# Optimization experiments

Measured on AMD Instinct MI355X. Metric: run time of the kernel, lower is better.

Reference implementation:

```python
import jax, jax.numpy as jnp
import numpy as np

N = 65536
WAVE_SPEED = 1.0


def _mlp(pt, Ws, bs):
    # pt: [4] -> scalar. 6 tanh hidden layers of width 128, linear head.
    h = pt
    for W, b in zip(Ws[:-1], bs[:-1]):
        h = jnp.tanh(W @ h + b)
    return (Ws[-1] @ h + bs[-1])[0]


def setup_inputs() -> dict:
    key = jax.random.key(0)
    ks = jax.random.split(key, 32)
    d = {}
    for i, name in enumerate(["t", "x", "y", "z"]):
        d[name] = jax.random.normal(ks[i], (N,), dtype=jnp.float32)
    sizes = [(128, 4)] + [(128, 128)] * 5 + [(1, 128)]
    for i, (fan_out, fan_in) in enumerate(sizes):
        # Glorot-like scale for tanh MLP
        scale = np.float32(1.0 / np.sqrt(fan_in))
        d[f"W{i}"] = jax.random.normal(ks[4 + i], (fan_out, fan_in), dtype=jnp.float32) * scale
        d[f"b{i}"] = jnp.zeros((fan_out,), dtype=jnp.float32)
    return d


def reference(t, x, y, z, W0, b0, W1, b1, W2, b2, W3, b3, W4, b4, W5, b5, W6, b6):
    Ws = [W0, W1, W2, W3, W4, W5, W6]
    bs = [b0, b1, b2, b3, b4, b5, b6]

    def u(pt):
        return _mlp(pt, Ws, bs)

    def residual_point(pt):
        # Full 4x4 Hessian via forward-over-reverse; we need only the diagonal.
        H = jax.hessian(u)(pt)  # [4, 4]
        u_tt = H[0, 0]
        laplacian = H[1, 1] + H[2, 2] + H[3, 3]
        return u_tt - (WAVE_SPEED ** 2) * laplacian

    pts = jnp.stack([t, x, y, z], axis=-1)  # [N, 4]
    return jax.vmap(residual_point)(pts)  # [N]
```

## Files before the change

kernel.cpp:

```cpp
#include <hip/hip_runtime.h>
#include <hip/hip_fp16.h>
#include <math.h>


typedef _Float16 f16x8 __attribute__((ext_vector_type(8)));
typedef _Float16 f16x4 __attribute__((ext_vector_type(4)));
typedef _Float16 f16x2 __attribute__((ext_vector_type(2)));
typedef float    f32x4 __attribute__((ext_vector_type(4)));

constexpr int TPB  = 256;
constexpr int P    = 16;
constexpr int H    = 128;
constexpr int NV   = 6;
constexpr int XFRAG_HALVES = NV * 4 * 64 * 8;
constexpr int WFRAG_HALVES = 5 * 8 * 4 * 64 * 8;
constexpr size_t WS_NEEDED = 2 * WFRAG_HALVES * sizeof(_Float16);

__device__ __forceinline__ float fast_tanh(float v) {
    float e = __expf(-2.0f * fabsf(v));
    float r = __builtin_amdgcn_rcpf(1.0f + e);
    return copysignf((1.0f - e) * r, v);
}

__device__ __forceinline__ f16x2 pkrtz(float a, float b) {
    return __builtin_bit_cast(f16x2, __builtin_amdgcn_cvt_pkrtz(a, b));
}

__global__ __launch_bounds__(256) void presplit_w(
    const float* __restrict__ W1, const float* __restrict__ W2,
    const float* __restrict__ W3, const float* __restrict__ W4,
    const float* __restrict__ W5, _Float16* __restrict__ whi,
    _Float16* __restrict__ wlo)
{
    const int gid = blockIdx.x * 256 + threadIdx.x;
    const float* Ws[5] = { W1, W2, W3, W4, W5 };
    const int lane = gid & 63;
    const int rest = gid >> 6;
    const int ks   = rest & 3;
    const int mt   = (rest >> 2) & 7;
    const int l    = rest >> 5;
    const int n    = mt * 16 + (lane & 15);
    const int k0   = ks * 32 + (lane >> 4) * 8;
    const float4 u0 = *(const float4*)&Ws[l][n * H + k0];
    const float4 u1 = *(const float4*)&Ws[l][n * H + k0 + 4];
    const float vv[8] = { u0.x, u0.y, u0.z, u0.w, u1.x, u1.y, u1.z, u1.w };
    f16x8 h, o;
    #pragma unroll
    for (int e = 0; e < 8; ++e) {
        _Float16 hh = (_Float16)vv[e];
        h[e] = hh;
        o[e] = (_Float16)(vv[e] - (float)hh);
    }
    *(f16x8*)&whi[gid * 8] = h;
    *(f16x8*)&wlo[gid * 8] = o;
}

__global__ __launch_bounds__(TPB, 3) void pinn_mfma8(
    const float* __restrict__ t, const float* __restrict__ x,
    const float* __restrict__ y, const float* __restrict__ z,
    const float* __restrict__ W0, const float* __restrict__ b0,
    const float* __restrict__ W1, const float* __restrict__ b1,
    const float* __restrict__ W2, const float* __restrict__ b2,
    const float* __restrict__ W3, const float* __restrict__ b3,
    const float* __restrict__ W4, const float* __restrict__ b4,
    const float* __restrict__ W5, const float* __restrict__ b5,
    const float* __restrict__ W6,
    const _Float16* __restrict__ whi, const _Float16* __restrict__ wlo,
    int use_pre, float* __restrict__ out, int N)
{
    __shared__ _Float16 sXhi[XFRAG_HALVES];
    __shared__ _Float16 sXlo[XFRAG_HALVES];
    __shared__ float    sRed[4][P];

    const int tid  = threadIdx.x;
    const int lane = tid & 63;
    const int wn   = tid >> 6;
    const int l15  = lane & 15;
    const int l4   = lane >> 4;
    const int gb   = blockIdx.x * P;

    {
        const int p0 = tid >> 4;
        const int i0 = tid & 15;
        int gp = gb + p0; if (gp >= N) gp = N - 1;
        const float pt0 = t[gp], pt1 = x[gp], pt2 = y[gp], pt3 = z[gp];
        float nv[NV][8];
        #pragma unroll
        for (int j = 0; j < 8; ++j) {
            const int i = i0 * 8 + j;
            const float4 wv = *(const float4*)&W0[i * 4];
            const float zv = fmaf(wv.x, pt0, fmaf(wv.y, pt1, fmaf(wv.z, pt2, fmaf(wv.w, pt3, b0[i]))));
            const float hv = fast_tanh(zv);
            const float s  = 1.0f - hv * hv;
            const float ssq = ((wv.x * wv.x - wv.y * wv.y) - wv.z * wv.z) - wv.w * wv.w;
            nv[0][j] = hv;       nv[1][j] = s * wv.x; nv[2][j] = s * wv.y;
            nv[3][j] = s * wv.z; nv[4][j] = s * wv.w; nv[5][j] = -2.0f * hv * s * ssq;
        }
        #pragma unroll
        for (int v = 0; v < NV; ++v) {
            f16x8 hh, oo;
            #pragma unroll
            for (int j = 0; j < 8; ++j) {
                _Float16 h_ = (_Float16)nv[v][j];
                hh[j] = h_;
                oo[j] = (_Float16)(nv[v][j] - (float)h_);
            }
            const int off = ((v * 4 + (i0 >> 2)) * 64 + p0 + 16 * (i0 & 3)) * 8;
            *(f16x8*)&sXhi[off] = hh;
            *(f16x8*)&sXlo[off] = oo;
        }
    }
    __syncthreads();

    for (int l = 0; l < 5; ++l) {
        f32x4 acc[NV][2];
        #pragma unroll
        for (int v = 0; v < NV; ++v)
            #pragma unroll
            for (int nt = 0; nt < 2; ++nt) acc[v][nt] = (f32x4){0.f, 0.f, 0.f, 0.f};

        const float* __restrict__ Wc =
            (l == 0) ? W1 : (l == 1) ? W2 : (l == 2) ? W3 : (l == 3) ? W4 : W5;

        #pragma unroll
        for (int ks = 0; ks < 4; ++ks) {
            f16x8 ah[2], al[2];
            if (use_pre) {
                #pragma unroll
                for (int nt = 0; nt < 2; ++nt) {
                    const int f = ((l * 8 + (wn * 2 + nt)) * 4 + ks) * 64 + lane;
                    ah[nt] = *(const f16x8*)&whi[f * 8];
                    al[nt] = *(const f16x8*)&wlo[f * 8];
                }
            } else {
                #pragma unroll
                for (int nt = 0; nt < 2; ++nt) {
                    const int n  = (wn * 2 + nt) * 16 + l15;
                    const int k0 = ks * 32 + l4 * 8;
                    const float4 u0 = *(const float4*)&Wc[n * H + k0];
                    const float4 u1 = *(const float4*)&Wc[n * H + k0 + 4];
                    const float vv[8] = { u0.x, u0.y, u0.z, u0.w, u1.x, u1.y, u1.z, u1.w };
                    #pragma unroll
                    for (int e = 0; e < 8; ++e) {
                        _Float16 h_ = (_Float16)vv[e];
                        ah[nt][e] = h_;
                        al[nt][e] = (_Float16)(vv[e] - (float)h_);
                    }
                }
            }
            f16x8 xh[NV], xl[NV];
            #pragma unroll
            for (int v = 0; v < NV; ++v) {
                const int base = ((v * 4 + ks) * 64 + lane) * 8;
                xh[v] = *(const f16x8*)&sXhi[base];
                xl[v] = *(const f16x8*)&sXlo[base];
            }
            __builtin_amdgcn_s_setprio(1);
            #pragma unroll
            for (int v = 0; v < NV; ++v)
                #pragma unroll
                for (int nt = 0; nt < 2; ++nt)
                    acc[v][nt] = __builtin_amdgcn_mfma_f32_16x16x32_f16(ah[nt], xh[v], acc[v][nt], 0, 0, 0);
            #pragma unroll
            for (int v = 0; v < NV; ++v)
                #pragma unroll
                for (int nt = 0; nt < 2; ++nt)
                    acc[v][nt] = __builtin_amdgcn_mfma_f32_16x16x32_f16(ah[nt], xl[v], acc[v][nt], 0, 0, 0);
            #pragma unroll
            for (int v = 0; v < NV; ++v)
                #pragma unroll
                for (int nt = 0; nt < 2; ++nt)
                    acc[v][nt] = __builtin_amdgcn_mfma_f32_16x16x32_f16(al[nt], xh[v], acc[v][nt], 0, 0, 0);
            __builtin_amdgcn_s_setprio(0);
        }
        __syncthreads();

        if (l < 4) {
            const float* __restrict__ bc =
                (l == 0) ? b1 : (l == 1) ? b2 : (l == 2) ? b3 : b4;
            #pragma unroll
            for (int nt = 0; nt < 2; ++nt) {
                const int n0  = (wn * 2 + nt) * 16 + l4 * 4;
                const int ksp = n0 >> 5;
                const int l4p = (n0 & 31) >> 3;
                const int e0  = n0 & 7;
                const float4 b4v = *(const float4*)&bc[n0];
                const float bb[4] = { b4v.x, b4v.y, b4v.z, b4v.w };
                float nv[NV][4];
                #pragma unroll
                for (int r = 0; r < 4; ++r) {
                    const float zv = acc[0][nt][r] + bb[r];
                    const float hv = fast_tanh(zv);
                    const float s  = 1.0f - hv * hv;
                    const float d0 = acc[1][nt][r], d1 = acc[2][nt][r];
                    const float d2 = acc[3][nt][r], d3 = acc[4][nt][r];
                    const float ssq = ((d0 * d0 - d1 * d1) - d2 * d2) - d3 * d3;
                    const float qn  = fmaf(s, acc[5][nt][r], -2.0f * hv * s * ssq);
                    nv[0][r] = hv;     nv[1][r] = s * d0; nv[2][r] = s * d1;
                    nv[3][r] = s * d2; nv[4][r] = s * d3; nv[5][r] = qn;
                }
                #pragma unroll
                for (int v = 0; v < NV; ++v) {
                    const f16x2 h01 = pkrtz(nv[v][0], nv[v][1]);
                    const f16x2 h23 = pkrtz(nv[v][2], nv[v][3]);
                    const float o0 = nv[v][0] - (float)h01[0];
                    const float o1 = nv[v][1] - (float)h01[1];
                    const float o2 = nv[v][2] - (float)h23[0];
                    const float o3 = nv[v][3] - (float)h23[1];
                    const f16x2 o01 = pkrtz(o0, o1);
                    const f16x2 o23 = pkrtz(o2, o3);
                    const int off = ((v * 4 + ksp) * 64 + l15 + 16 * l4p) * 8 + e0;
                    *(f16x4*)&sXhi[off] = __builtin_shufflevector(h01, h23, 0, 1, 2, 3);
                    *(f16x4*)&sXlo[off] = __builtin_shufflevector(o01, o23, 0, 1, 2, 3);
                }
            }
            __syncthreads();
        } else {
            float part = 0.0f;
            #pragma unroll
            for (int nt = 0; nt < 2; ++nt) {
                const int n0 = (wn * 2 + nt) * 16 + l4 * 4;
                const float4 b4v = *(const float4*)&b5[n0];
                const float4 w6v = *(const float4*)&W6[n0];
                const float bb[4] = { b4v.x, b4v.y, b4v.z, b4v.w };
                const float ww[4] = { w6v.x, w6v.y, w6v.z, w6v.w };
                #pragma unroll
                for (int r = 0; r < 4; ++r) {
                    const float zv = acc[0][nt][r] + bb[r];
                    const float hv = fast_tanh(zv);
                    const float s  = 1.0f - hv * hv;
                    const float d0 = acc[1][nt][r], d1 = acc[2][nt][r];
                    const float d2 = acc[3][nt][r], d3 = acc[4][nt][r];
                    const float ssq = ((d0 * d0 - d1 * d1) - d2 * d2) - d3 * d3;
                    const float qf  = fmaf(s, acc[5][nt][r], -2.0f * hv * s * ssq);
                    part = fmaf(ww[r], qf, part);
                }
            }
            part += __shfl_xor(part, 16, 64);
            part += __shfl_xor(part, 32, 64);
            if (lane < 16) sRed[wn][lane] = part;
        }
    }

    __syncthreads();
    if (tid < P) {
        const float rsum = sRed[0][tid] + sRed[1][tid] + sRed[2][tid] + sRed[3][tid];
        const int o = gb + tid;
        if (o < N) out[o] = rsum;
    }
}

extern "C" void kernel_launch(void* const* d_in, const int* in_sizes, int n_in,
                              void* d_out, int out_size, void* d_ws, size_t ws_size,
                              hipStream_t stream) {
    const float* t  = (const float*)d_in[0];
    const float* x  = (const float*)d_in[1];
    const float* y  = (const float*)d_in[2];
    const float* z  = (const float*)d_in[3];
    const float* W0 = (const float*)d_in[4];
    const float* b0 = (const float*)d_in[5];
    const float* W1 = (const float*)d_in[6];
    const float* b1 = (const float*)d_in[7];
    const float* W2 = (const float*)d_in[8];
    const float* b2 = (const float*)d_in[9];
    const float* W3 = (const float*)d_in[10];
    const float* b3 = (const float*)d_in[11];
    const float* W4 = (const float*)d_in[12];
    const float* b4 = (const float*)d_in[13];
    const float* W5 = (const float*)d_in[14];
    const float* b5 = (const float*)d_in[15];
    const float* W6 = (const float*)d_in[16];

    const int N = in_sizes[0];
    float* out = (float*)d_out;

    const int use_pre = (ws_size >= WS_NEEDED) ? 1 : 0;
    _Float16* whi = (_Float16*)d_ws;
    _Float16* wlo = whi + WFRAG_HALVES;

    if (use_pre) {
        presplit_w<<<(5 * 8 * 4 * 64) / 256, 256, 0, stream>>>(W1, W2, W3, W4, W5, whi, wlo);
    }
    const int grid = (N + P - 1) / P;
    pinn_mfma8<<<grid, TPB, 0, stream>>>(
        t, x, y, z, W0, b0, W1, b1, W2, b2, W3, b3, W4, b4, W5, b5, W6,
        whi, wlo, use_pre, out, N);
}
```

Measured before the change: 177.1 us.

## Pack two points' tangent vectors per MFMA column to halve blocks' accumulators

Each block now handles 8 points instead of 16. The six per-point tangent vectors (value, four first derivatives, second-derivative term) are interleaved so that each 16-wide MFMA N-tile holds 3 tiles × 2 channels per point, with even and odd columns carrying different channels. The cross-channel terms are recombined through lane-pair shuffles. This cuts the accumulator count from 12 to 6 f32x4, which frees registers and raises occupancy, with launch bounds going from 3 to 5 blocks per SIMD. The cost is twice as many blocks, which reload the weights more often per point, plus extra shuffles and select logic in the epilogue.

```diff
diff --git a/kernel.cpp b/kernel.cpp
--- a/kernel.cpp
+++ b/kernel.cpp
@@ -9,10 +9,11 @@
 typedef float    f32x4 __attribute__((ext_vector_type(4)));
 
 constexpr int TPB  = 256;
-constexpr int P    = 16;
+constexpr int P    = 8;
 constexpr int H    = 128;
 constexpr int NV   = 6;
-constexpr int XFRAG_HALVES = NV * 4 * 64 * 8;
+constexpr int NT   = 3;
+constexpr int XFRAG_HALVES = NT * 4 * 64 * 8;
 constexpr int WFRAG_HALVES = 5 * 8 * 4 * 64 * 8;
 constexpr size_t WS_NEEDED = 2 * WFRAG_HALVES * sizeof(_Float16);
 
@@ -55,7 +56,7 @@
     *(f16x8*)&wlo[gid * 8] = o;
 }
 
-__global__ __launch_bounds__(TPB, 3) void pinn_mfma8(
+__global__ __launch_bounds__(TPB, 5) void pinn_mfma10(
     const float* __restrict__ t, const float* __restrict__ x,
     const float* __restrict__ y, const float* __restrict__ z,
     const float* __restrict__ W0, const float* __restrict__ b0,
@@ -77,17 +78,18 @@
     const int wn   = tid >> 6;
     const int l15  = lane & 15;
     const int l4   = lane >> 4;
+    const int vo   = lane & 1;
     const int gb   = blockIdx.x * P;
 
     {
-        const int p0 = tid >> 4;
-        const int i0 = tid & 15;
+        const int p0 = tid >> 5;
+        const int i0 = tid & 31;
         int gp = gb + p0; if (gp >= N) gp = N - 1;
         const float pt0 = t[gp], pt1 = x[gp], pt2 = y[gp], pt3 = z[gp];
-        float nv[NV][8];
-        #pragma unroll
-        for (int j = 0; j < 8; ++j) {
-            const int i = i0 * 8 + j;
+        float nv[NV][4];
+        #pragma unroll
+        for (int j = 0; j < 4; ++j) {
+            const int i = i0 * 4 + j;
             const float4 wv = *(const float4*)&W0[i * 4];
             const float zv = fmaf(wv.x, pt0, fmaf(wv.y, pt1, fmaf(wv.z, pt2, fmaf(wv.w, pt3, b0[i]))));
             const float hv = fast_tanh(zv);
@@ -98,26 +100,28 @@
         }
         #pragma unroll
         for (int v = 0; v < NV; ++v) {
-            f16x8 hh, oo;
-            #pragma unroll
-            for (int j = 0; j < 8; ++j) {
+            f16x4 hh, oo;
+            #pragma unroll
+            for (int j = 0; j < 4; ++j) {
                 _Float16 h_ = (_Float16)nv[v][j];
                 hh[j] = h_;
                 oo[j] = (_Float16)(nv[v][j] - (float)h_);
             }
-            const int off = ((v * 4 + (i0 >> 2)) * 64 + p0 + 16 * (i0 & 3)) * 8;
-            *(f16x8*)&sXhi[off] = hh;
-            *(f16x8*)&sXlo[off] = oo;
+            const int off = (((v >> 1) * 4 + (i0 >> 3)) * 64
+                             + 16 * ((i0 >> 1) & 3) + 2 * p0 + (v & 1)) * 8
+                            + (i0 & 1) * 4;
+            *(f16x4*)&sXhi[off] = hh;
+            *(f16x4*)&sXlo[off] = oo;
         }
     }
     __syncthreads();
 
     for (int l = 0; l < 5; ++l) {
-        f32x4 acc[NV][2];
-        #pragma unroll
-        for (int v = 0; v < NV; ++v)
-            #pragma unroll
-            for (int nt = 0; nt < 2; ++nt) acc[v][nt] = (f32x4){0.f, 0.f, 0.f, 0.f};
+        f32x4 acc[NT][2];
+        #pragma unroll
+        for (int nt = 0; nt < NT; ++nt)
+            #pragma unroll
+            for (int m = 0; m < 2; ++m) acc[nt][m] = (f32x4){0.f, 0.f, 0.f, 0.f};
 
         const float* __restrict__ Wc =
             (l == 0) ? W1 : (l == 1) ? W2 : (l == 2) ? W3 : (l == 3) ? W4 : W5;
@@ -127,15 +131,15 @@
             f16x8 ah[2], al[2];
             if (use_pre) {
                 #pragma unroll
-                for (int nt = 0; nt < 2; ++nt) {
-                    const int f = ((l * 8 + (wn * 2 + nt)) * 4 + ks) * 64 + lane;
-                    ah[nt] = *(const f16x8*)&whi[f * 8];
-                    al[nt] = *(const f16x8*)&wlo[f * 8];
+                for (int m = 0; m < 2; ++m) {
+                    const int f = ((l * 8 + (wn * 2 + m)) * 4 + ks) * 64 + lane;
+                    ah[m] = *(const f16x8*)&whi[f * 8];
+                    al[m] = *(const f16x8*)&wlo[f * 8];
                 }
             } else {
                 #pragma unroll
-                for (int nt = 0; nt < 2; ++nt) {
-                    const int n  = (wn * 2 + nt) * 16 + l15;
+                for (int m = 0; m < 2; ++m) {
+                    const int n  = (wn * 2 + m) * 16 + l15;
                     const int k0 = ks * 32 + l4 * 8;
                     const float4 u0 = *(const float4*)&Wc[n * H + k0];
                     const float4 u1 = *(const float4*)&Wc[n * H + k0 + 4];
@@ -143,34 +147,34 @@
                     #pragma unroll
                     for (int e = 0; e < 8; ++e) {
                         _Float16 h_ = (_Float16)vv[e];
-                        ah[nt][e] = h_;
-                        al[nt][e] = (_Float16)(vv[e] - (float)h_);
+                        ah[m][e] = h_;
+                        al[m][e] = (_Float16)(vv[e] - (float)h_);
                     }
                 }
             }
-            f16x8 xh[NV], xl[NV];
-            #pragma unroll
-            for (int v = 0; v < NV; ++v) {
-                const int base = ((v * 4 + ks) * 64 + lane) * 8;
-                xh[v] = *(const f16x8*)&sXhi[base];
-                xl[v] = *(const f16x8*)&sXlo[base];
+            f16x8 xh[NT], xl[NT];
+            #pragma unroll
+            for (int nt = 0; nt < NT; ++nt) {
+                const int base = ((nt * 4 + ks) * 64 + lane) * 8;
+                xh[nt] = *(const f16x8*)&sXhi[base];
+                xl[nt] = *(const f16x8*)&sXlo[base];
             }
             __builtin_amdgcn_s_setprio(1);
             #pragma unroll
-            for (int v = 0; v < NV; ++v)
-                #pragma unroll
-                for (int nt = 0; nt < 2; ++nt)
-                    acc[v][nt] = __builtin_amdgcn_mfma_f32_16x16x32_f16(ah[nt], xh[v], acc[v][nt], 0, 0, 0);
-            #pragma unroll
-            for (int v = 0; v < NV; ++v)
-                #pragma unroll
-                for (int nt = 0; nt < 2; ++nt)
-                    acc[v][nt] = __builtin_amdgcn_mfma_f32_16x16x32_f16(ah[nt], xl[v], acc[v][nt], 0, 0, 0);
-            #pragma unroll
-            for (int v = 0; v < NV; ++v)
-                #pragma unroll
-                for (int nt = 0; nt < 2; ++nt)
-                    acc[v][nt] = __builtin_amdgcn_mfma_f32_16x16x32_f16(al[nt], xh[v], acc[v][nt], 0, 0, 0);
+            for (int nt = 0; nt < NT; ++nt)
+                #pragma unroll
+                for (int m = 0; m < 2; ++m)
+                    acc[nt][m] = __builtin_amdgcn_mfma_f32_16x16x32_f16(ah[m], xh[nt], acc[nt][m], 0, 0, 0);
+            #pragma unroll
+            for (int nt = 0; nt < NT; ++nt)
+                #pragma unroll
+                for (int m = 0; m < 2; ++m)
+                    acc[nt][m] = __builtin_amdgcn_mfma_f32_16x16x32_f16(ah[m], xl[nt], acc[nt][m], 0, 0, 0);
+            #pragma unroll
+            for (int nt = 0; nt < NT; ++nt)
+                #pragma unroll
+                for (int m = 0; m < 2; ++m)
+                    acc[nt][m] = __builtin_amdgcn_mfma_f32_16x16x32_f16(al[m], xh[nt], acc[nt][m], 0, 0, 0);
             __builtin_amdgcn_s_setprio(0);
         }
         __syncthreads();
@@ -179,66 +183,73 @@
             const float* __restrict__ bc =
                 (l == 0) ? b1 : (l == 1) ? b2 : (l == 2) ? b3 : b4;
             #pragma unroll
-            for (int nt = 0; nt < 2; ++nt) {
-                const int n0  = (wn * 2 + nt) * 16 + l4 * 4;
-                const int ksp = n0 >> 5;
-                const int l4p = (n0 & 31) >> 3;
-                const int e0  = n0 & 7;
-                const float4 b4v = *(const float4*)&bc[n0];
-                const float bb[4] = { b4v.x, b4v.y, b4v.z, b4v.w };
-                float nv[NV][4];
+            for (int m = 0; m < 2; ++m) {
+                float o0[4], o1[4], o2[4];
                 #pragma unroll
                 for (int r = 0; r < 4; ++r) {
-                    const float zv = acc[0][nt][r] + bb[r];
-                    const float hv = fast_tanh(zv);
-                    const float s  = 1.0f - hv * hv;
-                    const float d0 = acc[1][nt][r], d1 = acc[2][nt][r];
-                    const float d2 = acc[3][nt][r], d3 = acc[4][nt][r];
-                    const float ssq = ((d0 * d0 - d1 * d1) - d2 * d2) - d3 * d3;
-                    const float qn  = fmaf(s, acc[5][nt][r], -2.0f * hv * s * ssq);
-                    nv[0][r] = hv;     nv[1][r] = s * d0; nv[2][r] = s * d1;
-                    nv[3][r] = s * d2; nv[4][r] = s * d3; nv[5][r] = qn;
-                }
-                #pragma unroll
-                for (int v = 0; v < NV; ++v) {
-                    const f16x2 h01 = pkrtz(nv[v][0], nv[v][1]);
-                    const f16x2 h23 = pkrtz(nv[v][2], nv[v][3]);
-                    const float o0 = nv[v][0] - (float)h01[0];
-                    const float o1 = nv[v][1] - (float)h01[1];
-                    const float o2 = nv[v][2] - (float)h23[0];
-                    const float o3 = nv[v][3] - (float)h23[1];
-                    const f16x2 o01 = pkrtz(o0, o1);
-                    const f16x2 o23 = pkrtz(o2, o3);
-                    const int off = ((v * 4 + ksp) * 64 + l15 + 16 * l4p) * 8 + e0;
+                    const int n  = (wn * 2 + m) * 16 + l4 * 4 + r;
+                    const float a0 = acc[0][m][r];
+                    const float a1 = acc[1][m][r];
+                    const float a2 = acc[2][m][r];
+                    const float hv  = fast_tanh(a0 + bc[n]);
+                    const float s   = 1.0f - hv * hv;
+                    const float ue  = a1 * a1 + a2 * a2;
+                    const float hs2 = 2.0f * hv * s;
+                    const float s_x   = __shfl_xor(s, 1, 64);
+                    const float hs2_x = __shfl_xor(hs2, 1, 64);
+                    const float ue_x  = __shfl_xor(ue, 1, 64);
+                    const float uo  = a0 * a0 - a1 * a1;
+                    const float ssq = uo - ue_x;
+                    const float qn  = fmaf(s_x, a2, -hs2_x * ssq);
+                    o0[r] = vo ? s_x * a0 : hv;
+                    o1[r] = vo ? s_x * a1 : s * a1;
+                    o2[r] = vo ? qn       : s * a2;
+                }
+                const int wbase = 16 * (2 * m + (l4 >> 1)) + l15;
+                const int e0    = (l4 & 1) * 4;
+                #pragma unroll
+                for (int nt = 0; nt < NT; ++nt) {
+                    const float* ov = (nt == 0) ? o0 : (nt == 1) ? o1 : o2;
+                    const f16x2 h01 = pkrtz(ov[0], ov[1]);
+                    const f16x2 h23 = pkrtz(ov[2], ov[3]);
+                    const float q0 = ov[0] - (float)h01[0];
+                    const float q1 = ov[1] - (float)h01[1];
+                    const float q2 = ov[2] - (float)h23[0];
+                    const float q3 = ov[3] - (float)h23[1];
+                    const f16x2 g01 = pkrtz(q0, q1);
+                    const f16x2 g23 = pkrtz(q2, q3);
+                    const int off = ((nt * 4 + wn) * 64 + wbase) * 8 + e0;
                     *(f16x4*)&sXhi[off] = __builtin_shufflevector(h01, h23, 0, 1, 2, 3);
-                    *(f16x4*)&sXlo[off] = __builtin_shufflevector(o01, o23, 0, 1, 2, 3);
+                    *(f16x4*)&sXlo[off] = __builtin_shufflevector(g01, g23, 0, 1, 2, 3);
                 }
             }
             __syncthreads();
         } else {
             float part = 0.0f;
             #pragma unroll
-            for (int nt = 0; nt < 2; ++nt) {
-                const int n0 = (wn * 2 + nt) * 16 + l4 * 4;
-                const float4 b4v = *(const float4*)&b5[n0];
-                const float4 w6v = *(const float4*)&W6[n0];
-                const float bb[4] = { b4v.x, b4v.y, b4v.z, b4v.w };
-                const float ww[4] = { w6v.x, w6v.y, w6v.z, w6v.w };
+            for (int m = 0; m < 2; ++m) {
                 #pragma unroll
                 for (int r = 0; r < 4; ++r) {
-                    const float zv = acc[0][nt][r] + bb[r];
-                    const float hv = fast_tanh(zv);
-                    const float s  = 1.0f - hv * hv;
-                    const float d0 = acc[1][nt][r], d1 = acc[2][nt][r];
-                    const float d2 = acc[3][nt][r], d3 = acc[4][nt][r];
-                    const float ssq = ((d0 * d0 - d1 * d1) - d2 * d2) - d3 * d3;
-                    const float qf  = fmaf(s, acc[5][nt][r], -2.0f * hv * s * ssq);
-                    part = fmaf(ww[r], qf, part);
+                    const int n  = (wn * 2 + m) * 16 + l4 * 4 + r;
+                    const float a0 = acc[0][m][r];
+                    const float a1 = acc[1][m][r];
+                    const float a2 = acc[2][m][r];
+                    const float hv  = fast_tanh(a0 + b5[n]);
+                    const float s   = 1.0f - hv * hv;
+                    const float ue  = a1 * a1 + a2 * a2;
+                    const float hs2 = 2.0f * hv * s;
+                    const float s_x   = __shfl_xor(s, 1, 64);
+                    const float hs2_x = __shfl_xor(hs2, 1, 64);
+                    const float ue_x  = __shfl_xor(ue, 1, 64);
+                    const float uo  = a0 * a0 - a1 * a1;
+                    const float ssq = uo - ue_x;
+                    const float qf  = fmaf(s_x, a2, -hs2_x * ssq);
+                    part = fmaf(W6[n], qf, part);
                 }
             }
             part += __shfl_xor(part, 16, 64);
             part += __shfl_xor(part, 32, 64);
-            if (lane < 16) sRed[wn][lane] = part;
+            if (lane < 16 && (lane & 1)) sRed[wn][lane >> 1] = part;
         }
     }
 
@@ -282,7 +293,7 @@
         presplit_w<<<(5 * 8 * 4 * 64) / 256, 256, 0, stream>>>(W1, W2, W3, W4, W5, whi, wlo);
     }
     const int grid = (N + P - 1) / P;
-    pinn_mfma8<<<grid, TPB, 0, stream>>>(
+    pinn_mfma10<<<grid, TPB, 0, stream>>>(
         t, x, y, z, W0, b0, W1, b1, W2, b2, W3, b3, W4, b4, W5, b5, W6,
         whi, wlo, use_pre, out, N);
 }
```

Measured after the change: 227.0 us. +28.2%, slower.
